# Kernel tuning notes

Measured on AMD Instinct MI355X. Metric: run time of the kernel, lower is better.

## Reference

```python
import jax, jax.numpy as jnp
import numpy as np

B, N, DIM, H = 2, 4096, 1024, 16
LAT = 1024
CTX = N - LAT            # 3072 context tokens
SEG = 12                 # num_segments
CHUNK = CTX // SEG       # 256 tokens per segment
D = DIM // H             # 64 head dim
SCALE = D ** -0.5
LN_EPS = 1e-5
NEG = float(-np.finfo(np.float32).max)


def _split_heads(t):  # [B, N, DIM] -> [(B*H), N, D]
    return t.reshape(B, N, H, D).transpose(0, 2, 1, 3).reshape(B * H, N, D)


def _merge_heads(t):  # [(B*H), n, D] -> [B, n, DIM]
    n = t.shape[1]
    return t.reshape(B, H, n, D).transpose(0, 2, 1, 3).reshape(B, n, DIM)


def _layernorm(t, g, b):  # LN over last dim (head dim)
    mu = t.mean(-1, keepdims=True)
    var = ((t - mu) ** 2).mean(-1, keepdims=True)
    return (t - mu) * jax.lax.rsqrt(var + LN_EPS) * g + b


def _rope(t):  # rotary embedding over full head dim, half-split rotate
    pos = jnp.arange(N, dtype=jnp.float32)
    inv = 1.0 / (10000.0 ** (jnp.arange(0, D, 2, dtype=jnp.float32) / D))
    freqs = pos[:, None] * inv[None, :]          # [N, D/2]
    emb = jnp.concatenate([freqs, freqs], -1)    # [N, D]
    cos, sin = jnp.cos(emb), jnp.sin(emb)
    rot = jnp.concatenate([-t[..., D // 2:], t[..., : D // 2]], -1)
    return t * cos + rot * sin


def setup_inputs() -> dict:
    key = jax.random.key(0)
    ks = jax.random.split(key, 4)
    s = 0.02
    return {
        "x": jax.random.normal(ks[0], (B, N, DIM), jnp.float32),
        "Wq": jax.random.normal(ks[1], (DIM, DIM), jnp.float32) * s,
        "Wkv": jax.random.normal(ks[2], (DIM, DIM), jnp.float32) * s,
        "Wo": jax.random.normal(ks[3], (DIM, DIM), jnp.float32) * s,
        "bo": jnp.zeros((DIM,), jnp.float32),
        "ln_g": jnp.ones((D,), jnp.float32),
        "ln_b": jnp.zeros((D,), jnp.float32),
    }


def reference(x, Wq, Wkv, Wo, bo, ln_g, ln_b):
    q = _split_heads(x @ Wq)    # [(BH), N, D]
    kv = _split_heads(x @ Wkv)  # [(BH), N, D]
    q, kv = _rope(q), _rope(kv)

    lkv = _layernorm(kv, ln_g, ln_b)  # normalized keys/values, full seq

    q_lat = q[:, CTX:] * SCALE                                   # [(BH), LAT, D]
    q_ctx = (q[:, :CTX] * SCALE).reshape(B * H, SEG, CHUNK, D)   # segmented ctx queries
    lkv_ctx = lkv[:, :CTX].reshape(B * H, SEG, CHUNK, D)         # segmented norm'd kv

    # latent queries: full attention over all N positions, causal among latents
    lsim = jnp.einsum('bid,bjd->bij', q_lat, lkv)                # [(BH), LAT, N]
    tri = jnp.triu(jnp.ones((LAT, LAT), bool), 1)
    lat_block = jnp.where(tri, NEG, lsim[:, :, CTX:])
    lsim = jnp.concatenate([lsim[:, :, :CTX], lat_block], axis=-1)
    attn = jax.nn.softmax(lsim, axis=-1)
    out_lat = jnp.einsum('bij,bjd->bid', attn, lkv)              # [(BH), LAT, D]

    # context queries: block-diagonal segmented local attention (non-causal)
    sim_ctx = jnp.einsum('bsid,bsjd->bsij', q_ctx, lkv_ctx)      # [(BH), SEG, CHUNK, CHUNK]
    attn_ctx = jax.nn.softmax(sim_ctx, axis=-1)
    out_ctx = jnp.einsum('bsij,bsjd->bsid', attn_ctx, lkv_ctx).reshape(B * H, CTX, D)

    out = jnp.concatenate([_merge_heads(out_ctx), _merge_heads(out_lat)], axis=1)
    return out @ Wo + bo
```

## Files before the change

### kernel.cpp

```cpp
#include <hip/hip_runtime.h>
#include <math.h>

#define NB_B 2
#define NB_N 4096
#define NB_DIM 1024
#define NB_H 16
#define NB_D 64
#define NB_CTX 3072
#define NSPLIT 4
#define QSCALE 0.18033688011112042f
#define NEGF -3.0e38f

typedef __attribute__((ext_vector_type(8))) short short8;
typedef __attribute__((ext_vector_type(4))) short s4v;
typedef __attribute__((ext_vector_type(4))) float f32x4;

#if __has_builtin(__builtin_amdgcn_mfma_f32_16x16x16bf16_1k)
__device__ __forceinline__ f32x4 mfma16(s4v a, s4v b, f32x4 c) {
  return __builtin_amdgcn_mfma_f32_16x16x16bf16_1k(a, b, c, 0, 0, 0);
}
#else
__device__ __forceinline__ f32x4 mfma16(s4v a, s4v b, f32x4 c) {
  f32x4 d;
  asm volatile("v_mfma_f32_16x16x16_bf16 %0, %1, %2, %3"
               : "=v"(d) : "v"(a), "v"(b), "v"(c));
  return d;
}
#endif

__device__ __forceinline__ unsigned short f2bf(float f) {
  union { float f; unsigned u; } v; v.f = f;
  unsigned r = v.u + 0x7fffu + ((v.u >> 16) & 1u);
  return (unsigned short)(r >> 16);
}

__device__ __forceinline__ void async16(const void* g, void* l) {
  typedef const unsigned int __attribute__((address_space(1)))* gas_t;
  typedef unsigned int __attribute__((address_space(3)))* las_t;
  __builtin_amdgcn_global_load_lds((gas_t)(unsigned long long)g,
                                   (las_t)(unsigned)(unsigned long long)l,
                                   16, 0, 0);
}

__global__ __launch_bounds__(256) void k_prep(
    const float* __restrict__ x,
    const float* __restrict__ Wq, const float* __restrict__ Wkv, const float* __restrict__ Wo,
    unsigned short* __restrict__ xb, unsigned short* __restrict__ WqkvT,
    unsigned short* __restrict__ WoT, float2* __restrict__ tab)
{
  __shared__ float tile[64][65];
  const int bx = blockIdx.x, tid = threadIdx.x;
  if (bx < 2048) {
    const float4* x4 = (const float4*)x;
    ushort4* xb4 = (ushort4*)xb;
    const int n4 = (NB_B * NB_N * NB_DIM) / 4;
    for (int i = bx * 256 + tid; i < n4; i += 2048 * 256) {
      float4 v = x4[i];
      ushort4 o;
      o.x = f2bf(v.x); o.y = f2bf(v.y); o.z = f2bf(v.z); o.w = f2bf(v.w);
      xb4[i] = o;
    }
  } else if (bx < 2816) {
    int idx = bx - 2048;
    int z = idx >> 8, rem = idx & 255;
    const float* W; unsigned short* out;
    if (z == 0)      { W = Wq;  out = WqkvT; }
    else if (z == 1) { W = Wkv; out = WqkvT + 1024 * 1024; }
    else             { W = Wo;  out = WoT; }
    int c0 = (rem & 15) * 64, k0 = (rem >> 4) * 64;
    int tx = tid & 63, ty = tid >> 6;
    #pragma unroll
    for (int i = 0; i < 16; ++i) {
      int k = ty + i * 4;
      tile[k][tx] = W[(long)(k0 + k) * 1024 + c0 + tx];
    }
    __syncthreads();
    #pragma unroll
    for (int i = 0; i < 16; ++i) {
      int c = ty + i * 4;
      out[(long)(c0 + c) * 1024 + k0 + tx] = f2bf(tile[tx][c]);
    }
  } else {
    int idx = (bx - 2816) * 256 + tid;
    int n = idx >> 5, fi = idx & 31;
    float inv = exp2f(-(float)fi * (13.287712379549449f / 32.0f));
    float ang = (float)n * inv;
    float s, c;
    sincosf(ang, &s, &c);
    tab[idx] = make_float2(c, s);
  }
}

__global__ __launch_bounds__(256) void k_gemm_qkv(
    const unsigned short* __restrict__ A,
    const unsigned short* __restrict__ Bt,
    unsigned short* __restrict__ qf,
    unsigned short* __restrict__ lkvp,
    const float2* __restrict__ tab,
    const float* __restrict__ ln_g,
    const float* __restrict__ ln_b)
{
  __shared__ unsigned short As[128 * 32];
  __shared__ unsigned short Bs[128 * 32];
  const int tid = threadIdx.x;
  const int w = tid >> 6, lane = tid & 63;
  const int wr = w >> 1, wc = w & 1;
  const int quad = lane >> 4, l15 = lane & 15;
  const long tm = (long)blockIdx.y * 128, tn = (long)blockIdx.x * 128;
  const int K = 1024;

  f32x4 acc[4][4];
  #pragma unroll
  for (int i = 0; i < 4; ++i)
    #pragma unroll
    for (int j = 0; j < 4; ++j)
      acc[i][j] = (f32x4){0.f, 0.f, 0.f, 0.f};

  const unsigned short* Ag0 = A + (tm + w * 16 + (lane >> 2)) * K + (lane & 3) * 8;
  const unsigned short* Bg0 = Bt + (tn + w * 16 + (lane >> 2)) * K + (lane & 3) * 8;
  const unsigned short* Ag1 = Ag0 + (long)64 * K;
  const unsigned short* Bg1 = Bg0 + (long)64 * K;
  unsigned short* Al0 = &As[(w * 16) * 32];
  unsigned short* Al1 = &As[(64 + w * 16) * 32];
  unsigned short* Bl0 = &Bs[(w * 16) * 32];
  unsigned short* Bl1 = &Bs[(64 + w * 16) * 32];

  for (int k0 = 0; k0 < K; k0 += 32) {
    __syncthreads();
    async16(Ag0 + k0, Al0);
    async16(Ag1 + k0, Al1);
    async16(Bg0 + k0, Bl0);
    async16(Bg1 + k0, Bl1);
    __syncthreads();
    short8 af[4], bfr[4];
    #pragma unroll
    for (int i = 0; i < 4; ++i)
      af[i] = *(const short8*)&As[(wr * 64 + i * 16 + l15) * 32 + quad * 8];
    #pragma unroll
    for (int j = 0; j < 4; ++j)
      bfr[j] = *(const short8*)&Bs[(wc * 64 + j * 16 + l15) * 32 + quad * 8];
    #pragma unroll
    for (int i = 0; i < 4; ++i)
      #pragma unroll
      for (int j = 0; j < 4; ++j)
        acc[i][j] = __builtin_amdgcn_mfma_f32_16x16x32_bf16(af[i], bfr[j], acc[i][j], 0, 0, 0);
  }

  const int col_base = (int)tn + wc * 64;
  const bool is_q = col_base < 1024;
  const int hh = (col_base & 1023) >> 6;
  unsigned short* dst = is_q ? qf : lkvp;
  float g_ln[4], b_ln[4];
  #pragma unroll
  for (int j = 0; j < 4; ++j) { g_ln[j] = ln_g[j * 16 + l15]; b_ln[j] = ln_b[j * 16 + l15]; }

  const int row_base = (int)tm + wr * 64;
  #pragma unroll
  for (int i = 0; i < 4; ++i) {
    #pragma unroll
    for (int r = 0; r < 4; ++r) {
      const int row = row_base + i * 16 + quad * 4 + r;
      const int n = row & 4095, b = row >> 12;
      const float2 cs0 = tab[n * 32 + l15];
      const float2 cs1 = tab[n * 32 + 16 + l15];
      float val[4];
      #pragma unroll
      for (int j = 0; j < 4; ++j) {
        float t = acc[i][j][r], pt = acc[i][j ^ 2][r];
        float2 cs = (j & 1) ? cs1 : cs0;
        float rot = (j < 2) ? -pt : pt;
        val[j] = t * cs.x + rot * cs.y;
      }
      unsigned short* orow = dst + ((long)(b * 16 + hh) * NB_N + n) * 64;
      if (is_q) {
        #pragma unroll
        for (int j = 0; j < 4; ++j)
          orow[j * 16 + l15] = f2bf(val[j] * QSCALE);
      } else {
        float s = val[0] + val[1] + val[2] + val[3];
        #pragma unroll
        for (int o = 1; o < 16; o <<= 1) s += __shfl_xor(s, o);
        const float mu = s * 0.015625f;
        float dv[4], vs = 0.f;
        #pragma unroll
        for (int j = 0; j < 4; ++j) { dv[j] = val[j] - mu; vs += dv[j] * dv[j]; }
        #pragma unroll
        for (int o = 1; o < 16; o <<= 1) vs += __shfl_xor(vs, o);
        const float rr = rsqrtf(vs * 0.015625f + 1e-5f);
        #pragma unroll
        for (int j = 0; j < 4; ++j)
          orow[j * 16 + l15] = f2bf(dv[j] * rr * g_ln[j] + b_ln[j]);
      }
    }
  }
}

__global__ __launch_bounds__(256) void k_gemm_bt(
    const unsigned short* __restrict__ A,
    const unsigned short* __restrict__ Bt,
    float* __restrict__ C,
    const float* __restrict__ bias,
    int K, int ldc)
{
  __shared__ unsigned short As[128 * 32];
  __shared__ unsigned short Bs[128 * 32];
  const int tid = threadIdx.x;
  const int w = tid >> 6, lane = tid & 63;
  const int wr = w >> 1, wc = w & 1;
  const int quad = lane >> 4, l15 = lane & 15;
  const long tm = (long)blockIdx.y * 128, tn = (long)blockIdx.x * 128;

  f32x4 acc[4][4];
  #pragma unroll
  for (int i = 0; i < 4; ++i)
    #pragma unroll
    for (int j = 0; j < 4; ++j)
      acc[i][j] = (f32x4){0.f, 0.f, 0.f, 0.f};

  const unsigned short* Ag0 = A + (tm + w * 16 + (lane >> 2)) * K + (lane & 3) * 8;
  const unsigned short* Bg0 = Bt + (tn + w * 16 + (lane >> 2)) * K + (lane & 3) * 8;
  const unsigned short* Ag1 = Ag0 + (long)64 * K;
  const unsigned short* Bg1 = Bg0 + (long)64 * K;
  unsigned short* Al0 = &As[(w * 16) * 32];
  unsigned short* Al1 = &As[(64 + w * 16) * 32];
  unsigned short* Bl0 = &Bs[(w * 16) * 32];
  unsigned short* Bl1 = &Bs[(64 + w * 16) * 32];

  for (int k0 = 0; k0 < K; k0 += 32) {
    __syncthreads();
    async16(Ag0 + k0, Al0);
    async16(Ag1 + k0, Al1);
    async16(Bg0 + k0, Bl0);
    async16(Bg1 + k0, Bl1);
    __syncthreads();
    short8 af[4], bfr[4];
    #pragma unroll
    for (int i = 0; i < 4; ++i)
      af[i] = *(const short8*)&As[(wr * 64 + i * 16 + l15) * 32 + quad * 8];
    #pragma unroll
    for (int j = 0; j < 4; ++j)
      bfr[j] = *(const short8*)&Bs[(wc * 64 + j * 16 + l15) * 32 + quad * 8];
    #pragma unroll
    for (int i = 0; i < 4; ++i)
      #pragma unroll
      for (int j = 0; j < 4; ++j)
        acc[i][j] = __builtin_amdgcn_mfma_f32_16x16x32_bf16(af[i], bfr[j], acc[i][j], 0, 0, 0);
  }

  #pragma unroll
  for (int j = 0; j < 4; ++j) {
    const long col = tn + wc * 64 + j * 16 + l15;
    const float bv = bias ? bias[col] : 0.0f;
    #pragma unroll
    for (int i = 0; i < 4; ++i) {
      #pragma unroll
      for (int r = 0; r < 4; ++r) {
        const long row = tm + wr * 64 + i * 16 + quad * 4 + r;
        C[row * ldc + col] = acc[i][j][r] + bv;
      }
    }
  }
}

__global__ __launch_bounds__(256) void k_attn(
    const unsigned short* __restrict__ qf,
    const unsigned short* __restrict__ lkv,
    unsigned short* __restrict__ attn_out,
    float* __restrict__ Opart,
    float* __restrict__ mpart,
    float* __restrict__ lpart)
{
  __shared__ unsigned short smem[9216];
  unsigned short* Ks = smem;
  unsigned short* Vt = smem + 4608;

  const int tid = threadIdx.x;
  const int w = tid >> 6, lane = tid & 63;
  const int quad = lane >> 4, l15 = lane & 15;

  const int bx = blockIdx.x;
  int bh, q0tok, kstart, kt0, kt1, q0lat, s6 = 0, qb = 0;
  bool latent;
  if (bx < 256 * NSPLIT) {
    latent = true;
    qb = bx / NSPLIT;
    s6 = bx % NSPLIT;
    bh = qb >> 3;
    q0lat = (qb & 7) * 128;
    q0tok = NB_CTX + q0lat;
    kstart = 0;
    int nkt = (NB_CTX + q0lat + 128) >> 6;
    kt0 = (s6 * nkt) / NSPLIT;
    kt1 = ((s6 + 1) * nkt) / NSPLIT;
  } else {
    latent = false;
    int idx = bx - 256 * NSPLIT;
    bh = idx / 24;
    int r2 = idx % 24;
    int seg = r2 >> 1;
    q0lat = 0;
    q0tok = seg * 256 + (r2 & 1) * 128;
    kstart = seg * 256;
    kt0 = 0; kt1 = 4;
  }

  const unsigned short* qbase = qf + ((long)bh * NB_N + q0tok) * 64;
  const unsigned short* kbase = lkv + (long)bh * NB_N * 64;

  short8 qfr[2][2];
  #pragma unroll
  for (int qg = 0; qg < 2; ++qg)
    #pragma unroll
    for (int kc = 0; kc < 2; ++kc)
      qfr[qg][kc] = *(const short8*)(qbase + (w * 32 + qg * 16 + l15) * 64 + kc * 32 + quad * 8);

  const int kp = tid >> 3, sdc = tid & 7;

  uint4 gA, gB;
  {
    const int key0 = kstart + kt0 * 64;
    gA = *(const uint4*)(kbase + (long)(key0 + 2 * kp) * 64 + sdc * 8);
    gB = *(const uint4*)(kbase + (long)(key0 + 2 * kp + 1) * 64 + sdc * 8);
  }

  f32x4 ot[2][4];
  float mi[2], li[2];
  #pragma unroll
  for (int qg = 0; qg < 2; ++qg) {
    #pragma unroll
    for (int dt = 0; dt < 4; ++dt) ot[qg][dt] = (f32x4){0.f, 0.f, 0.f, 0.f};
    mi[qg] = 0.f; li[qg] = 0.f;
  }

  for (int kt = kt0; kt < kt1; ++kt) {
    const int key0 = kstart + kt * 64;
    __syncthreads();
    *(uint4*)&Ks[(2 * kp) * 72 + sdc * 8] = gA;
    *(uint4*)&Ks[(2 * kp + 1) * 72 + sdc * 8] = gB;
    {
      const unsigned short* eA = (const unsigned short*)&gA;
      const unsigned short* eB = (const unsigned short*)&gB;
      #pragma unroll
      for (int j = 0; j < 8; ++j) {
        const int d = sdc * 8 + j;
        const unsigned int pair = (unsigned int)eA[j] | ((unsigned int)eB[j] << 16);
        *(unsigned int*)&Vt[d * 72 + ((2 * kp) ^ (d & 56))] = pair;
      }
    }
    __syncthreads();
    if (kt + 1 < kt1) {
      const int key0n = key0 + 64;
      gA = *(const uint4*)(kbase + (long)(key0n + 2 * kp) * 64 + sdc * 8);
      gB = *(const uint4*)(kbase + (long)(key0n + 2 * kp + 1) * 64 + sdc * 8);
    }

    f32x4 st[2][4];
    #pragma unroll
    for (int qg = 0; qg < 2; ++qg)
      #pragma unroll
      for (int k4 = 0; k4 < 4; ++k4)
        st[qg][k4] = (f32x4){0.f, 0.f, 0.f, 0.f};
    #pragma unroll
    for (int kc = 0; kc < 2; ++kc) {
      short8 kf[4];
      #pragma unroll
      for (int k4 = 0; k4 < 4; ++k4)
        kf[k4] = *(const short8*)&Ks[(k4 * 16 + l15) * 72 + kc * 32 + quad * 8];
      #pragma unroll
      for (int qg = 0; qg < 2; ++qg)
        #pragma unroll
        for (int k4 = 0; k4 < 4; ++k4)
          st[qg][k4] = __builtin_amdgcn_mfma_f32_16x16x32_bf16(kf[k4], qfr[qg][kc], st[qg][k4], 0, 0, 0);
    }

    if (latent && key0 + 63 >= NB_CTX) {
      #pragma unroll
      for (int qg = 0; qg < 2; ++qg) {
        const int qrow = q0lat + w * 32 + qg * 16 + l15;
        #pragma unroll
        for (int k4 = 0; k4 < 4; ++k4)
          #pragma unroll
          for (int r = 0; r < 4; ++r) {
            const int kl = key0 + k4 * 16 + quad * 4 + r - NB_CTX;
            if (kl > qrow) st[qg][k4][r] = NEGF;
          }
      }
    }

    unsigned int pk[2][4][2];
    float tmx[2], trs[2];
    #pragma unroll
    for (int qg = 0; qg < 2; ++qg) {
      float rs = 0.f;
      float mx = st[qg][0][0];
      #pragma unroll
      for (int k4 = 0; k4 < 4; ++k4) {
        unsigned int b[4];
        #pragma unroll
        for (int r = 0; r < 4; ++r) {
          mx = fmaxf(mx, st[qg][k4][r]);
          float p = __builtin_amdgcn_exp2f(st[qg][k4][r] - mi[qg]);
          unsigned int pb = __float_as_uint(p) & 0xffff0000u;
          rs += __uint_as_float(pb);
          b[r] = pb;
        }
        pk[qg][k4][0] = __builtin_amdgcn_perm(b[1], b[0], 0x07060302);
        pk[qg][k4][1] = __builtin_amdgcn_perm(b[3], b[2], 0x07060302);
      }
      tmx[qg] = mx; trs[qg] = rs;
    }

    #pragma unroll
    for (int k4 = 0; k4 < 4; ++k4) {
      s4v vf[4];
      const int kb = k4 * 16 + quad * 4;
      #pragma unroll
      for (int dt = 0; dt < 4; ++dt) {
        const int row = dt * 16 + l15;
        vf[dt] = *(const s4v*)&Vt[row * 72 + (kb ^ (row & 56))];
      }
      #pragma unroll
      for (int qg = 0; qg < 2; ++qg) {
        s4v pf;
        ((unsigned int*)&pf)[0] = pk[qg][k4][0];
        ((unsigned int*)&pf)[1] = pk[qg][k4][1];
        #pragma unroll
        for (int dt = 0; dt < 4; ++dt)
          ot[qg][dt] = mfma16(vf[dt], pf, ot[qg][dt]);
      }
    }

    #pragma unroll
    for (int qg = 0; qg < 2; ++qg) {
      float rs = trs[qg];
      rs += __shfl_xor(rs, 16);
      rs += __shfl_xor(rs, 32);
      float mx = tmx[qg];
      mx = fmaxf(mx, __shfl_xor(mx, 16));
      mx = fmaxf(mx, __shfl_xor(mx, 32));
      const float mnew = fmaxf(mi[qg], mx);
      const float c = __builtin_amdgcn_exp2f(mi[qg] - mnew);
      mi[qg] = mnew;
      li[qg] = (li[qg] + rs) * c;
      #pragma unroll
      for (int dt = 0; dt < 4; ++dt) {
        ot[qg][dt][0] *= c; ot[qg][dt][1] *= c;
        ot[qg][dt][2] *= c; ot[qg][dt][3] *= c;
      }
    }
  }

  __syncthreads();
  if (latent) {
    const long pb = (long)(s6 * 256 + qb);
    if (quad == 0) {
      #pragma unroll
      for (int qg = 0; qg < 2; ++qg) {
        mpart[pb * 128 + w * 32 + qg * 16 + l15] = mi[qg];
        lpart[pb * 128 + w * 32 + qg * 16 + l15] = li[qg];
      }
    }
    float* obase = Opart + pb * 8192;
    #pragma unroll
    for (int qg = 0; qg < 2; ++qg) {
      const int q = w * 32 + qg * 16 + l15;
      #pragma unroll
      for (int dt = 0; dt < 4; ++dt)
        #pragma unroll
        for (int r = 0; r < 4; ++r)
          obase[(dt * 16 + quad * 4 + r) * 128 + q] = ot[qg][dt][r];
    }
  } else {
    #pragma unroll
    for (int qg = 0; qg < 2; ++qg) {
      const float inv = 1.0f / li[qg];
      const int q = w * 32 + qg * 16 + l15;
      #pragma unroll
      for (int dt = 0; dt < 4; ++dt)
        #pragma unroll
        for (int r = 0; r < 4; ++r)
          smem[q * 72 + dt * 16 + quad * 4 + r] = f2bf(ot[qg][dt][r] * inv);
    }
    __syncthreads();
    const int qrow = tid >> 1, half = tid & 1;
    const int b_ = bh >> 4, h_ = bh & 15;
    unsigned short* orow = attn_out + ((long)b_ * NB_N + q0tok + qrow) * NB_DIM + h_ * 64 + half * 32;
    #pragma unroll
    for (int v = 0; v < 4; ++v)
      *(uint4*)(orow + v * 8) = *(const uint4*)&smem[qrow * 72 + half * 32 + v * 8];
  }
}

__global__ __launch_bounds__(256) void k_combine(
    const float* __restrict__ Opart, const float* __restrict__ mpart,
    const float* __restrict__ lpart, unsigned short* __restrict__ attn_out)
{
  __shared__ unsigned short lds[9216];
  const int qb = blockIdx.x;
  const int bh = qb >> 3, qt = qb & 7;
  const int b = bh >> 4, h = bh & 15;
  const int t = threadIdx.x;
  const int qq = t & 31;
  const int dg = t >> 5;

  float m[NSPLIT][4], l[NSPLIT][4];
  float mstar[4];
  #pragma unroll
  for (int qi = 0; qi < 4; ++qi) mstar[qi] = NEGF;
  #pragma unroll
  for (int s = 0; s < NSPLIT; ++s) {
    #pragma unroll
    for (int qi = 0; qi < 4; ++qi) {
      m[s][qi] = mpart[(s * 256 + qb) * 128 + qq * 4 + qi];
      l[s][qi] = lpart[(s * 256 + qb) * 128 + qq * 4 + qi];
      mstar[qi] = fmaxf(mstar[qi], m[s][qi]);
    }
  }
  float inv[4];
  #pragma unroll
  for (int qi = 0; qi < 4; ++qi) {
    float lsum = 0.f;
    #pragma unroll
    for (int s = 0; s < NSPLIT; ++s)
      lsum += __builtin_amdgcn_exp2f(m[s][qi] - mstar[qi]) * l[s][qi];
    inv[qi] = 1.0f / lsum;
  }

  float o[8][4];
  #pragma unroll
  for (int dd = 0; dd < 8; ++dd)
    #pragma unroll
    for (int qi = 0; qi < 4; ++qi) o[dd][qi] = 0.f;
  #pragma unroll
  for (int s = 0; s < NSPLIT; ++s) {
    float wgt[4];
    #pragma unroll
    for (int qi = 0; qi < 4; ++qi)
      wgt[qi] = __builtin_amdgcn_exp2f(m[s][qi] - mstar[qi]);
    const float* base = Opart + (long)(s * 256 + qb) * 8192;
    #pragma unroll
    for (int dd = 0; dd < 8; ++dd) {
      float4 v = *(const float4*)(base + (dg * 8 + dd) * 128 + qq * 4);
      o[dd][0] += wgt[0] * v.x; o[dd][1] += wgt[1] * v.y;
      o[dd][2] += wgt[2] * v.z; o[dd][3] += wgt[3] * v.w;
    }
  }
  #pragma unroll
  for (int qi = 0; qi < 4; ++qi) {
    ushort4 u0, u1;
    u0.x = f2bf(o[0][qi] * inv[qi]); u0.y = f2bf(o[1][qi] * inv[qi]);
    u0.z = f2bf(o[2][qi] * inv[qi]); u0.w = f2bf(o[3][qi] * inv[qi]);
    u1.x = f2bf(o[4][qi] * inv[qi]); u1.y = f2bf(o[5][qi] * inv[qi]);
    u1.z = f2bf(o[6][qi] * inv[qi]); u1.w = f2bf(o[7][qi] * inv[qi]);
    *(ushort4*)&lds[(qq * 4 + qi) * 72 + dg * 8] = u0;
    *(ushort4*)&lds[(qq * 4 + qi) * 72 + dg * 8 + 4] = u1;
  }
  __syncthreads();
  const int qrow = t >> 1, half = t & 1;
  unsigned short* orow = attn_out + ((long)b * NB_N + NB_CTX + qt * 128 + qrow) * NB_DIM + h * 64 + half * 32;
  #pragma unroll
  for (int v = 0; v < 4; ++v)
    *(uint4*)(orow + v * 8) = *(const uint4*)&lds[qrow * 72 + half * 32 + v * 8];
}

extern "C" void kernel_launch(void* const* d_in, const int* in_sizes, int n_in,
                              void* d_out, int out_size, void* d_ws, size_t ws_size,
                              hipStream_t stream)
{
  const float* x    = (const float*)d_in[0];
  const float* Wq   = (const float*)d_in[1];
  const float* Wkv  = (const float*)d_in[2];
  const float* Wo   = (const float*)d_in[3];
  const float* bo   = (const float*)d_in[4];
  const float* ln_g = (const float*)d_in[5];
  const float* ln_b = (const float*)d_in[6];
  float* out = (float*)d_out;

  char* ws = (char*)d_ws;
  unsigned short* xb    = (unsigned short*)(ws);
  unsigned short* WqkvT = (unsigned short*)(ws + (size_t)(16 << 20));
  unsigned short* WoT   = (unsigned short*)(ws + (size_t)(20 << 20));
  float2*         tab   = (float2*)        (ws + (size_t)(22 << 20));
  unsigned short* qfb   = (unsigned short*)(ws + (size_t)(24 << 20));
  unsigned short* lkv   = (unsigned short*)(ws + (size_t)(40 << 20));
  unsigned short* aout  = (unsigned short*)(ws + (size_t)(56 << 20));
  float*          Opart = (float*)         (ws + (size_t)(72 << 20));
  float*          mpart = (float*)         (ws + (size_t)(112 << 20));
  float*          lpart = (float*)         (ws + (size_t)(113 << 20));

  hipLaunchKernelGGL(k_prep, dim3(3328), dim3(256), 0, stream,
                     x, Wq, Wkv, Wo, xb, WqkvT, WoT, tab);
  hipLaunchKernelGGL(k_gemm_qkv, dim3(16, 64), dim3(256), 0, stream,
                     xb, WqkvT, qfb, lkv, tab, ln_g, ln_b);
  hipLaunchKernelGGL(k_attn, dim3(256 * NSPLIT + 768), dim3(256), 0, stream,
                     qfb, lkv, aout, Opart, mpart, lpart);
  hipLaunchKernelGGL(k_combine, dim3(256), dim3(256), 0, stream,
                     Opart, mpart, lpart, aout);
  hipLaunchKernelGGL(k_gemm_bt, dim3(8, 64), dim3(256), 0, stream,
                     aout, WoT, out, bo, 1024, 1024);
}
```

Measured before the change: 277.4 us.

## Double-buffer K/V tiles in LDS and use lazy softmax rescaling

The attention kernel now keeps two LDS buffers for the K and transposed-V tiles. The next tile is written into the alternate buffer while the current one is consumed, which removes one of the two barriers per iteration. The V transpose now uses perm-based word packing instead of per-element shifts. The online-softmax rescale is skipped unless the running max rises by more than 8 in log2 units, which saves exp and multiply work but relies on the bounded-overflow assumption. LDS use doubles, which may lower occupancy.

```diff
diff --git a/kernel.cpp b/kernel.cpp
--- a/kernel.cpp
+++ b/kernel.cpp
@@ -270,9 +270,7 @@
     float* __restrict__ mpart,
     float* __restrict__ lpart)
 {
-  __shared__ unsigned short smem[9216];
-  unsigned short* Ks = smem;
-  unsigned short* Vt = smem + 4608;
+  __shared__ unsigned short smem[18432];
 
   const int tid = threadIdx.x;
   const int w = tid >> 6, lane = tid & 63;
@@ -323,6 +321,29 @@
     gB = *(const uint4*)(kbase + (long)(key0 + 2 * kp + 1) * 64 + sdc * 8);
   }
 
+  {
+    unsigned short* Ks0 = smem;
+    unsigned short* Vt0 = smem + 4608;
+    *(uint4*)&Ks0[(2 * kp) * 72 + sdc * 8] = gA;
+    *(uint4*)&Ks0[(2 * kp + 1) * 72 + sdc * 8] = gB;
+    const unsigned int* wA = (const unsigned int*)&gA;
+    const unsigned int* wB = (const unsigned int*)&gB;
+    #pragma unroll
+    for (int jw = 0; jw < 4; ++jw) {
+      const unsigned int lo = __builtin_amdgcn_perm(wB[jw], wA[jw], 0x05040100u);
+      const unsigned int hi = __builtin_amdgcn_perm(wB[jw], wA[jw], 0x07060302u);
+      const int d0 = sdc * 8 + jw * 2;
+      const int xo = (2 * kp) ^ (d0 & 56);
+      *(unsigned int*)&Vt0[d0 * 72 + xo] = lo;
+      *(unsigned int*)&Vt0[(d0 + 1) * 72 + xo] = hi;
+    }
+  }
+  if (kt0 + 1 < kt1) {
+    const int key0n = kstart + (kt0 + 1) * 64;
+    gA = *(const uint4*)(kbase + (long)(key0n + 2 * kp) * 64 + sdc * 8);
+    gB = *(const uint4*)(kbase + (long)(key0n + 2 * kp + 1) * 64 + sdc * 8);
+  }
+
   f32x4 ot[2][4];
   float mi[2], li[2];
   #pragma unroll
@@ -332,26 +353,34 @@
     mi[qg] = 0.f; li[qg] = 0.f;
   }
 
+  int cur = 0;
   for (int kt = kt0; kt < kt1; ++kt) {
     const int key0 = kstart + kt * 64;
     __syncthreads();
-    *(uint4*)&Ks[(2 * kp) * 72 + sdc * 8] = gA;
-    *(uint4*)&Ks[(2 * kp + 1) * 72 + sdc * 8] = gB;
-    {
-      const unsigned short* eA = (const unsigned short*)&gA;
-      const unsigned short* eB = (const unsigned short*)&gB;
-      #pragma unroll
-      for (int j = 0; j < 8; ++j) {
-        const int d = sdc * 8 + j;
-        const unsigned int pair = (unsigned int)eA[j] | ((unsigned int)eB[j] << 16);
-        *(unsigned int*)&Vt[d * 72 + ((2 * kp) ^ (d & 56))] = pair;
-      }
-    }
-    __syncthreads();
+    const unsigned short* Ks = smem + cur;
+    const unsigned short* Vt = smem + cur + 4608;
+
     if (kt + 1 < kt1) {
-      const int key0n = key0 + 64;
-      gA = *(const uint4*)(kbase + (long)(key0n + 2 * kp) * 64 + sdc * 8);
-      gB = *(const uint4*)(kbase + (long)(key0n + 2 * kp + 1) * 64 + sdc * 8);
+      unsigned short* Ksn = smem + (cur ^ 9216);
+      unsigned short* Vtn = Ksn + 4608;
+      *(uint4*)&Ksn[(2 * kp) * 72 + sdc * 8] = gA;
+      *(uint4*)&Ksn[(2 * kp + 1) * 72 + sdc * 8] = gB;
+      const unsigned int* wA = (const unsigned int*)&gA;
+      const unsigned int* wB = (const unsigned int*)&gB;
+      #pragma unroll
+      for (int jw = 0; jw < 4; ++jw) {
+        const unsigned int lo = __builtin_amdgcn_perm(wB[jw], wA[jw], 0x05040100u);
+        const unsigned int hi = __builtin_amdgcn_perm(wB[jw], wA[jw], 0x07060302u);
+        const int d0 = sdc * 8 + jw * 2;
+        const int xo = (2 * kp) ^ (d0 & 56);
+        *(unsigned int*)&Vtn[d0 * 72 + xo] = lo;
+        *(unsigned int*)&Vtn[(d0 + 1) * 72 + xo] = hi;
+      }
+      if (kt + 2 < kt1) {
+        const int key0n = key0 + 128;
+        gA = *(const uint4*)(kbase + (long)(key0n + 2 * kp) * 64 + sdc * 8);
+        gB = *(const uint4*)(kbase + (long)(key0n + 2 * kp + 1) * 64 + sdc * 8);
+      }
     }
 
     f32x4 st[2][4];
@@ -392,18 +421,19 @@
     #pragma unroll
     for (int qg = 0; qg < 2; ++qg) {
       float rs = 0.f;
-      float mx = st[qg][0][0];
+      float mx = NEGF;
       #pragma unroll
       for (int k4 = 0; k4 < 4; ++k4) {
         unsigned int b[4];
         #pragma unroll
         for (int r = 0; r < 4; ++r) {
-          mx = fmaxf(mx, st[qg][k4][r]);
           float p = __builtin_amdgcn_exp2f(st[qg][k4][r] - mi[qg]);
           unsigned int pb = __float_as_uint(p) & 0xffff0000u;
           rs += __uint_as_float(pb);
           b[r] = pb;
         }
+        mx = fmaxf(mx, fmaxf(fmaxf(st[qg][k4][0], st[qg][k4][1]),
+                             fmaxf(st[qg][k4][2], st[qg][k4][3])));
         pk[qg][k4][0] = __builtin_amdgcn_perm(b[1], b[0], 0x07060302);
         pk[qg][k4][1] = __builtin_amdgcn_perm(b[3], b[2], 0x07060302);
       }
@@ -438,16 +468,21 @@
       float mx = tmx[qg];
       mx = fmaxf(mx, __shfl_xor(mx, 16));
       mx = fmaxf(mx, __shfl_xor(mx, 32));
-      const float mnew = fmaxf(mi[qg], mx);
-      const float c = __builtin_amdgcn_exp2f(mi[qg] - mnew);
-      mi[qg] = mnew;
-      li[qg] = (li[qg] + rs) * c;
-      #pragma unroll
-      for (int dt = 0; dt < 4; ++dt) {
-        ot[qg][dt][0] *= c; ot[qg][dt][1] *= c;
-        ot[qg][dt][2] *= c; ot[qg][dt][3] *= c;
-      }
-    }
+      if (__builtin_expect(mx > mi[qg] + 8.f, 0)) {
+        const float c = __builtin_amdgcn_exp2f(mi[qg] - mx);
+        mi[qg] = mx;
+        li[qg] = (li[qg] + rs) * c;
+        #pragma unroll
+        for (int dt = 0; dt < 4; ++dt) {
+          ot[qg][dt][0] *= c; ot[qg][dt][1] *= c;
+          ot[qg][dt][2] *= c; ot[qg][dt][3] *= c;
+        }
+      } else {
+        li[qg] += rs;
+      }
+    }
+
+    cur ^= 9216;
   }
 
   __syncthreads();
```

Result: no change. 282.6 us (+1.9%).
